# Kernel optimization log

Measured on AMD Instinct MI355X. Metric: run time of the kernel, lower is better.

The kernel has to match this reference:

```python
import jax, jax.numpy as jnp
import numpy as np

B, N, E, K = 8, 4096, 1, 3
F = [16, 32, 16]
MLP_HID, MLP_OUT = 64, 1


def graph_filter(x, S, h, b):
    # x: [B, Fin, N], S: [E, N, N], h: [Fout, E, K, Fin], b: [Fout, 1]
    Bx, Fin, Nx = x.shape
    Ex, Kx = h.shape[1], h.shape[2]
    cur = jnp.broadcast_to(x[:, None], (Bx, Ex, Fin, Nx))  # tap 0: z = x
    zs = [cur]
    for _ in range(Kx - 1):
        cur = jnp.einsum('enm,befm->befn', S, cur)  # diffuse one hop
        zs.append(cur)
    z = jnp.stack(zs, axis=2)  # [B, E, K, Fin, N]
    return jnp.einsum('gekf,bekfn->bgn', h, z) + b[None]  # [B, Fout, N]


def gnn_layer(x, S, h, b, n_out):
    # GraphFilter -> ReLU -> NoPool (select first n_out nodes)
    return jax.nn.relu(graph_filter(x, S, h, b))[:, :, :n_out]


def setup_inputs() -> dict:
    key = jax.random.key(0)
    ks = jax.random.split(key, 16)
    sN = np.float32(1.0 / np.sqrt(N))
    x = jax.random.normal(ks[0], (B, F[0], N), dtype=jnp.float32)
    S_clique = jax.random.normal(ks[1], (E, N, N), dtype=jnp.float32) * sN
    S_line = jax.random.normal(ks[2], (E, N, N), dtype=jnp.float32) * sN

    def w(k, fo, fi):
        s = np.float32(1.0 / np.sqrt(fi * K))
        return jax.random.normal(k, (fo, E, K, fi), dtype=jnp.float32) * s

    Wc1, bc1 = w(ks[3], F[1], F[0]), jnp.zeros((F[1], 1), jnp.float32)
    Wc2, bc2 = w(ks[4], F[2], F[1]), jnp.zeros((F[2], 1), jnp.float32)
    Wl1, bl1 = w(ks[5], F[1], F[0]), jnp.zeros((F[1], 1), jnp.float32)
    Wl2, bl2 = w(ks[6], F[2], F[1]), jnp.zeros((F[2], 1), jnp.float32)
    d_in = N * F[-1]
    Wm1 = jax.random.normal(ks[7], (MLP_HID, d_in), dtype=jnp.float32) * np.float32(1.0 / np.sqrt(d_in))
    bm1 = jnp.zeros((MLP_HID,), jnp.float32)
    Wm2 = jax.random.normal(ks[8], (MLP_OUT, MLP_HID), dtype=jnp.float32) * np.float32(1.0 / np.sqrt(MLP_HID))
    bm2 = jnp.zeros((MLP_OUT,), jnp.float32)
    return {'x': x, 'S_clique': S_clique, 'S_line': S_line,
            'Wc1': Wc1, 'bc1': bc1, 'Wc2': Wc2, 'bc2': bc2,
            'Wl1': Wl1, 'bl1': bl1, 'Wl2': Wl2, 'bl2': bl2,
            'Wm1': Wm1, 'bm1': bm1, 'Wm2': Wm2, 'bm2': bm2}


def reference(x, S_clique, S_line, Wc1, bc1, Wc2, bc2, Wl1, bl1, Wl2, bl2, Wm1, bm1, Wm2, bm2):
    # clique-expansion branch (L=2 layers)
    y = gnn_layer(x, S_clique, Wc1, bc1, N)
    y = gnn_layer(y, S_clique, Wc2, bc2, N)
    # line-expansion branch (L=2 layers)
    y = gnn_layer(y, S_line, Wl1, bl1, N)
    y = gnn_layer(y, S_line, Wl2, bl2, N)
    yFlat = y.reshape(y.shape[0], -1)  # [B, F[-1]*N] (row-major matches torch)
    h = jax.nn.relu(yFlat @ Wm1.T + bm1)
    return h @ Wm2.T + bm2  # [B, 1]
```

## Files before the change

### kernel.cpp

```cpp
#include <hip/hip_runtime.h>


#define NN 4096
#define BB 8

typedef unsigned short u16;
typedef unsigned int   u32;

typedef __attribute__((ext_vector_type(8))) short bf16x8;
typedef __attribute__((ext_vector_type(4))) float f32x4;

__device__ __forceinline__ u16 f2bf(float f) {
    union { float f; u32 i; } c; c.f = f;
    u32 i = c.i;
    u32 r = (i + 0x7FFFu + ((i >> 16) & 1u)) >> 16;
    return (u16)r;
}
__device__ __forceinline__ float bf2f(u16 u) {
    union { u32 i; float f; } c; c.i = ((u32)u) << 16; return c.f;
}

__device__ __forceinline__ void gload_lds16(const u16* g, u16* l) {
    __builtin_amdgcn_global_load_lds(
        (__attribute__((address_space(1))) void*)g,
        (__attribute__((address_space(3))) void*)l, 16, 0, 0);
}

__global__ __launch_bounds__(256) void cvt_f32_bf16(const float* __restrict__ in,
                                                    u16* __restrict__ out, int n)
{
    int i = (blockIdx.x * 256 + threadIdx.x) * 4;
    const int stride = gridDim.x * 256 * 4;
    for (; i < n; i += stride) {
        float4 v = *(const float4*)(in + i);
        ushort4 o;
        o.x = f2bf(v.x); o.y = f2bf(v.y); o.z = f2bf(v.z); o.w = f2bf(v.w);
        *(ushort4*)(out + i) = o;
    }
}

__global__ __launch_bounds__(256) void diffuse(const u16* __restrict__ Z,
                                               const u16* __restrict__ S,
                                               u16* __restrict__ Part)
{
    __shared__ u16 As[2][128 * 64];
    __shared__ u16 Bs[2][64 * 64];

    const int bx    = blockIdx.x;
    const int ntile = ((bx & 7) << 3) | (bx >> 3);
    const int nBase = ntile * 64;
    const int mBase = blockIdx.y * 128;
    const int tid   = threadIdx.x;
    const int lane  = tid & 63;
    const int wv    = tid >> 6;
    const int quad  = lane >> 4;
    const int l16   = lane & 15;

    const int kSlice = NN / (int)gridDim.z;
    const int kStart = (int)blockIdx.z * kSlice;
    const int iters  = kSlice / 64;

    const int rl   = lane >> 3;
    const int gsl  = lane & 7;
    const int gsrc = gsl ^ rl;

    f32x4 acc[2][4];
#pragma unroll
    for (int i = 0; i < 2; ++i)
#pragma unroll
        for (int j = 0; j < 4; ++j) acc[i][j] = (f32x4){0.f, 0.f, 0.f, 0.f};

    auto stage = [&](int buf, int k0) {
#pragma unroll
        for (int j = 0; j < 4; ++j) {
            const int rb = (wv * 4 + j) * 8;
            gload_lds16(Z + (size_t)(mBase + rb + rl) * NN + k0 + gsrc * 8,
                        &As[buf][rb * 64]);
        }
#pragma unroll
        for (int j = 0; j < 2; ++j) {
            const int rb = (wv * 2 + j) * 8;
            gload_lds16(S + (size_t)(nBase + rb + rl) * NN + k0 + gsrc * 8,
                        &Bs[buf][rb * 64]);
        }
    };

    auto compute = [&](int buf) {
#pragma unroll
        for (int s = 0; s < 2; ++s) {
            const int g = s * 4 + quad;
            bf16x8 af[2], bf[4];
#pragma unroll
            for (int mi = 0; mi < 2; ++mi) {
                const int r = wv * 32 + mi * 16 + l16;
                af[mi] = *(const bf16x8*)&As[buf][r * 64 + ((g ^ (r & 7)) << 3)];
            }
#pragma unroll
            for (int ni = 0; ni < 4; ++ni) {
                const int r = ni * 16 + l16;
                bf[ni] = *(const bf16x8*)&Bs[buf][r * 64 + ((g ^ (r & 7)) << 3)];
            }
#pragma unroll
            for (int mi = 0; mi < 2; ++mi)
#pragma unroll
                for (int ni = 0; ni < 4; ++ni)
                    acc[mi][ni] = __builtin_amdgcn_mfma_f32_16x16x32_bf16(
                        af[mi], bf[ni], acc[mi][ni], 0, 0, 0);
        }
    };

    stage(0, kStart);
    __syncthreads();

    int cur = 0;
    for (int i = 0; i < iters - 1; ++i) {
        stage(cur ^ 1, kStart + (i + 1) * 64);
        compute(cur);
        __syncthreads();
        cur ^= 1;
    }
    compute(cur);

    const size_t plane = (size_t)gridDim.y * 128 * NN;
    u16* pp = Part + (size_t)blockIdx.z * plane;
#pragma unroll
    for (int mi = 0; mi < 2; ++mi)
#pragma unroll
        for (int ni = 0; ni < 4; ++ni) {
            const int row0 = mBase + wv * 32 + mi * 16 + quad * 4;
            const int col  = nBase + ni * 16 + l16;
#pragma unroll
            for (int i = 0; i < 4; ++i)
                pp[(size_t)(row0 + i) * NN + col] = f2bf(acc[mi][ni][i]);
        }
}

template <int KS>
__global__ __launch_bounds__(256) void reduce_part(const u16* __restrict__ part,
                                                   int planeElems,
                                                   u16* __restrict__ outb)
{
    const int base   = (blockIdx.x * 256 + threadIdx.x) * 8;
    const int stride = gridDim.x * 256 * 8;
    for (int i = base; i < planeElems; i += stride) {
        float s[8];
#pragma unroll
        for (int e = 0; e < 8; ++e) s[e] = 0.f;
#pragma unroll
        for (int p = 0; p < KS; ++p) {
            uint4 v = *(const uint4*)(part + (size_t)p * planeElems + i);
            const u32 w[4] = {v.x, v.y, v.z, v.w};
#pragma unroll
            for (int q = 0; q < 4; ++q) {
                union { u32 i; float f; } lo, hi;
                lo.i = w[q] << 16;
                hi.i = w[q] & 0xFFFF0000u;
                s[q * 2]     += lo.f;
                s[q * 2 + 1] += hi.f;
            }
        }
        uint4 o;
        o.x = (u32)f2bf(s[0]) | ((u32)f2bf(s[1]) << 16);
        o.y = (u32)f2bf(s[2]) | ((u32)f2bf(s[3]) << 16);
        o.z = (u32)f2bf(s[4]) | ((u32)f2bf(s[5]) << 16);
        o.w = (u32)f2bf(s[6]) | ((u32)f2bf(s[7]) << 16);
        *(uint4*)(outb + i) = o;
    }
}

template <int FIN, int FOUT, int KS>
__global__ __launch_bounds__(256) void combine_relu(
    const u16* __restrict__ z0, const u16* __restrict__ z1,
    const u16* __restrict__ part2, int planeElems,
    const float* __restrict__ W, const float* __restrict__ bias,
    u16* __restrict__ out)
{
    __shared__ float hs[FOUT * 3 * FIN];
    __shared__ float bs[FOUT];
    for (int i = threadIdx.x; i < FOUT * 3 * FIN; i += 256) hs[i] = W[i];
    if (threadIdx.x < FOUT) bs[threadIdx.x] = bias[threadIdx.x];
    __syncthreads();

    const int nb = NN / 256;
    const int b  = blockIdx.x / nb;
    const int n  = (blockIdx.x % nb) * 256 + threadIdx.x;

    float zv[3][FIN];
    const u16* zp0 = z0 + (size_t)b * FIN * NN + n;
    const u16* zp1 = z1 + (size_t)b * FIN * NN + n;
    const u16* zp2 = part2 + (size_t)b * FIN * NN + n;
#pragma unroll
    for (int f = 0; f < FIN; ++f) {
        zv[0][f] = bf2f(zp0[(size_t)f * NN]);
        zv[1][f] = bf2f(zp1[(size_t)f * NN]);
        float s = 0.f;
#pragma unroll
        for (int p = 0; p < KS; ++p)
            s += bf2f(zp2[(size_t)p * planeElems + (size_t)f * NN]);
        zv[2][f] = s;
    }

    u16* op = out + (size_t)b * FOUT * NN + n;
    for (int g = 0; g < FOUT; ++g) {
        float acc = bs[g];
#pragma unroll
        for (int k = 0; k < 3; ++k)
#pragma unroll
            for (int f = 0; f < FIN; ++f)
                acc = fmaf(hs[(g * 3 + k) * FIN + f], zv[k][f], acc);
        op[(size_t)g * NN] = f2bf(fmaxf(acc, 0.f));
    }
}

__global__ __launch_bounds__(256) void mlp1(const u16* __restrict__ y,
                                            const float* __restrict__ Wm1,
                                            float* __restrict__ h1p)
{
    const int j    = blockIdx.x;
    const int base = blockIdx.y * 8192;
    const int D    = 16 * NN;

    float acc[BB];
#pragma unroll
    for (int b = 0; b < BB; ++b) acc[b] = 0.f;

    const float* wrow = Wm1 + (size_t)j * D + base;
    for (int idx = threadIdx.x * 8; idx < 8192; idx += 256 * 8) {
        float4 w0 = *(const float4*)(wrow + idx);
        float4 w1 = *(const float4*)(wrow + idx + 4);
#pragma unroll
        for (int b = 0; b < BB; ++b) {
            uint4 yv = *(const uint4*)(y + (size_t)b * D + base + idx);
            union { u32 i; float f; } c[8];
            c[0].i = yv.x << 16; c[1].i = yv.x & 0xFFFF0000u;
            c[2].i = yv.y << 16; c[3].i = yv.y & 0xFFFF0000u;
            c[4].i = yv.z << 16; c[5].i = yv.z & 0xFFFF0000u;
            c[6].i = yv.w << 16; c[7].i = yv.w & 0xFFFF0000u;
            acc[b] = fmaf(w0.x, c[0].f, acc[b]);
            acc[b] = fmaf(w0.y, c[1].f, acc[b]);
            acc[b] = fmaf(w0.z, c[2].f, acc[b]);
            acc[b] = fmaf(w0.w, c[3].f, acc[b]);
            acc[b] = fmaf(w1.x, c[4].f, acc[b]);
            acc[b] = fmaf(w1.y, c[5].f, acc[b]);
            acc[b] = fmaf(w1.z, c[6].f, acc[b]);
            acc[b] = fmaf(w1.w, c[7].f, acc[b]);
        }
    }

    __shared__ float red[BB][4];
    const int lane = threadIdx.x & 63;
    const int w    = threadIdx.x >> 6;
#pragma unroll
    for (int b = 0; b < BB; ++b) {
        float v = acc[b];
        for (int off = 32; off > 0; off >>= 1) v += __shfl_down(v, off, 64);
        if (lane == 0) red[b][w] = v;
    }
    __syncthreads();
    if (threadIdx.x < BB) {
        const int b = threadIdx.x;
        h1p[blockIdx.y * (BB * 64) + b * 64 + j] =
            red[b][0] + red[b][1] + red[b][2] + red[b][3];
    }
}

__global__ void mlp2(const float* __restrict__ h1p,
                     const float* __restrict__ bm1,
                     const float* __restrict__ Wm2,
                     const float* __restrict__ bm2, float* __restrict__ out)
{
    const int lane = threadIdx.x;
    const float w    = Wm2[lane];
    const float b1   = bm1[lane];
    const float bias = bm2[0];
    for (int b = 0; b < BB; ++b) {
        float h = 0.f;
#pragma unroll
        for (int p = 0; p < 8; ++p) h += h1p[p * (BB * 64) + b * 64 + lane];
        float v = fmaxf(h + b1, 0.f) * w;
        for (int off = 32; off > 0; off >>= 1) v += __shfl_down(v, off, 64);
        if (lane == 0) out[b] = v + bias;
    }
}

extern "C" void kernel_launch(void* const* d_in, const int* in_sizes, int n_in,
                              void* d_out, int out_size, void* d_ws, size_t ws_size,
                              hipStream_t stream)
{
    const float* x   = (const float*)d_in[0];
    const float* Sc  = (const float*)d_in[1];
    const float* Sl  = (const float*)d_in[2];
    const float* Wc1 = (const float*)d_in[3];
    const float* bc1 = (const float*)d_in[4];
    const float* Wc2 = (const float*)d_in[5];
    const float* bc2 = (const float*)d_in[6];
    const float* Wl1 = (const float*)d_in[7];
    const float* bl1 = (const float*)d_in[8];
    const float* Wl2 = (const float*)d_in[9];
    const float* bl2 = (const float*)d_in[10];
    const float* Wm1 = (const float*)d_in[11];
    const float* bm1 = (const float*)d_in[12];
    const float* Wm2 = (const float*)d_in[13];
    const float* bm2 = (const float*)d_in[14];
    float* out = (float*)d_out;

    char* ws = (char*)d_ws;
    u16*   part = (u16*)(ws);
    u16*   zb1  = (u16*)(ws + (8u  << 20));
    u16*   yPa  = (u16*)(ws + (12u << 20));
    u16*   yPb  = (u16*)(ws + (14u << 20));
    float* h1p  = (float*)(ws + (16u << 20));
    u16*   Scb  = (u16*)(ws + (17u << 20));
    u16*   Slb  = Scb + (size_t)NN * NN;

    const dim3 blk(256);
    const dim3 gridCmb(BB * NN / 256);
    const dim3 g2(64, 1, 8);
    const dim3 g4(64, 2, 4);
    const int  pl128 = 128 * NN;
    const int  pl256 = 256 * NN;

    cvt_f32_bf16<<<1024, blk, 0, stream>>>(Sc, Scb, NN * NN);
    cvt_f32_bf16<<<1024, blk, 0, stream>>>(Sl, Slb, NN * NN);
    cvt_f32_bf16<<<512, blk, 0, stream>>>(x, yPa, 128 * NN);

    diffuse<<<g2, blk, 0, stream>>>(yPa, Scb, part);
    reduce_part<8><<<256, blk, 0, stream>>>(part, pl128, zb1);
    diffuse<<<g2, blk, 0, stream>>>(zb1, Scb, part);
    combine_relu<16, 32, 8><<<gridCmb, blk, 0, stream>>>(yPa, zb1, part, pl128,
                                                         Wc1, bc1, yPb);
    diffuse<<<g4, blk, 0, stream>>>(yPb, Scb, part);
    reduce_part<4><<<512, blk, 0, stream>>>(part, pl256, zb1);
    diffuse<<<g4, blk, 0, stream>>>(zb1, Scb, part);
    combine_relu<32, 16, 4><<<gridCmb, blk, 0, stream>>>(yPb, zb1, part, pl256,
                                                         Wc2, bc2, yPa);
    diffuse<<<g2, blk, 0, stream>>>(yPa, Slb, part);
    reduce_part<8><<<256, blk, 0, stream>>>(part, pl128, zb1);
    diffuse<<<g2, blk, 0, stream>>>(zb1, Slb, part);
    combine_relu<16, 32, 8><<<gridCmb, blk, 0, stream>>>(yPa, zb1, part, pl128,
                                                         Wl1, bl1, yPb);
    diffuse<<<g4, blk, 0, stream>>>(yPb, Slb, part);
    reduce_part<4><<<512, blk, 0, stream>>>(part, pl256, zb1);
    diffuse<<<g4, blk, 0, stream>>>(zb1, Slb, part);
    combine_relu<32, 16, 4><<<gridCmb, blk, 0, stream>>>(yPb, zb1, part, pl256,
                                                         Wl2, bl2, yPa);
    mlp1<<<dim3(64, 8), blk, 0, stream>>>(yPa, Wm1, h1p);
    mlp2<<<1, 64, 0, stream>>>(h1p, bm1, Wm2, bm2, out);
}
```

Measured before the change: 388.0 us.

## Triple-buffer diffuse GEMM with vmcnt waits, LDS-staged stores, fused conversions

The diffuse GEMM moves from a double-buffered loop with __syncthreads to a three-stage LDS pipeline. It uses explicit s_waitcnt vmcnt counts and raw barriers, and the iteration count becomes a template parameter so the loop fully unrolls. The output tile is staged through LDS so partial results go out as 16-byte row-contiguous stores instead of scattered 2-byte writes. The three f32-to-bf16 conversion launches are merged into one kernel. The changes aim to hide global-load latency and cut store transactions and launch overhead, at the cost of more LDS per block (possible occupancy loss) and hand-counted waitcnt values that must match the number of issued loads.

After: 373.6 us. 3.7% less time.

```diff
diff --git a/kernel.cpp b/kernel.cpp
--- a/kernel.cpp
+++ b/kernel.cpp
@@ -26,25 +26,31 @@
         (__attribute__((address_space(3))) void*)l, 16, 0, 0);
 }
 
-__global__ __launch_bounds__(256) void cvt_f32_bf16(const float* __restrict__ in,
-                                                    u16* __restrict__ out, int n)
-{
-    int i = (blockIdx.x * 256 + threadIdx.x) * 4;
-    const int stride = gridDim.x * 256 * 4;
-    for (; i < n; i += stride) {
-        float4 v = *(const float4*)(in + i);
+__global__ __launch_bounds__(256) void cvt3(const float* __restrict__ a, u16* __restrict__ da, int na,
+                                            const float* __restrict__ b, u16* __restrict__ db, int nb,
+                                            const float* __restrict__ c, u16* __restrict__ dc, int nc)
+{
+    const int tot = (na + nb + nc) >> 2;
+    for (int q = blockIdx.x * 256 + threadIdx.x; q < tot; q += gridDim.x * 256) {
+        const int i = q << 2;
+        const float* s; u16* d;
+        if (i < na)           { s = a + i;            d = da + i; }
+        else if (i < na + nb) { s = b + (i - na);     d = db + (i - na); }
+        else                  { s = c + (i - na - nb); d = dc + (i - na - nb); }
+        float4 v = *(const float4*)s;
         ushort4 o;
         o.x = f2bf(v.x); o.y = f2bf(v.y); o.z = f2bf(v.z); o.w = f2bf(v.w);
-        *(ushort4*)(out + i) = o;
-    }
-}
-
+        *(ushort4*)d = o;
+    }
+}
+
+template <int ITERS>
 __global__ __launch_bounds__(256) void diffuse(const u16* __restrict__ Z,
                                                const u16* __restrict__ S,
                                                u16* __restrict__ Part)
 {
-    __shared__ u16 As[2][128 * 64];
-    __shared__ u16 Bs[2][64 * 64];
+    __shared__ u16 As[3 * 128 * 64];
+    __shared__ u16 Bs[3 * 64 * 64];
 
     const int bx    = blockIdx.x;
     const int ntile = ((bx & 7) << 3) | (bx >> 3);
@@ -56,9 +62,7 @@
     const int quad  = lane >> 4;
     const int l16   = lane & 15;
 
-    const int kSlice = NN / (int)gridDim.z;
-    const int kStart = (int)blockIdx.z * kSlice;
-    const int iters  = kSlice / 64;
+    const int kStart = (int)blockIdx.z * (ITERS * 64);
 
     const int rl   = lane >> 3;
     const int gsl  = lane & 7;
@@ -75,13 +79,13 @@
         for (int j = 0; j < 4; ++j) {
             const int rb = (wv * 4 + j) * 8;
             gload_lds16(Z + (size_t)(mBase + rb + rl) * NN + k0 + gsrc * 8,
-                        &As[buf][rb * 64]);
+                        &As[buf * 8192 + rb * 64]);
         }
 #pragma unroll
         for (int j = 0; j < 2; ++j) {
             const int rb = (wv * 2 + j) * 8;
             gload_lds16(S + (size_t)(nBase + rb + rl) * NN + k0 + gsrc * 8,
-                        &Bs[buf][rb * 64]);
+                        &Bs[buf * 4096 + rb * 64]);
         }
     };
 
@@ -93,12 +97,12 @@
 #pragma unroll
             for (int mi = 0; mi < 2; ++mi) {
                 const int r = wv * 32 + mi * 16 + l16;
-                af[mi] = *(const bf16x8*)&As[buf][r * 64 + ((g ^ (r & 7)) << 3)];
+                af[mi] = *(const bf16x8*)&As[buf * 8192 + r * 64 + ((g ^ (r & 7)) << 3)];
             }
 #pragma unroll
             for (int ni = 0; ni < 4; ++ni) {
                 const int r = ni * 16 + l16;
-                bf[ni] = *(const bf16x8*)&Bs[buf][r * 64 + ((g ^ (r & 7)) << 3)];
+                bf[ni] = *(const bf16x8*)&Bs[buf * 4096 + r * 64 + ((g ^ (r & 7)) << 3)];
             }
 #pragma unroll
             for (int mi = 0; mi < 2; ++mi)
@@ -110,29 +114,45 @@
     };
 
     stage(0, kStart);
-    __syncthreads();
-
-    int cur = 0;
-    for (int i = 0; i < iters - 1; ++i) {
-        stage(cur ^ 1, kStart + (i + 1) * 64);
-        compute(cur);
-        __syncthreads();
-        cur ^= 1;
-    }
-    compute(cur);
+    stage(1, kStart + 64);
+
+#pragma unroll
+    for (int i = 0; i < ITERS; ++i) {
+        if (i + 2 < ITERS) stage((i + 2) % 3, kStart + (i + 2) * 64);
+        if (i < ITERS - 2)
+            asm volatile("s_waitcnt vmcnt(12)" ::: "memory");
+        else if (i == ITERS - 2)
+            asm volatile("s_waitcnt vmcnt(6)" ::: "memory");
+        else
+            asm volatile("s_waitcnt vmcnt(0)" ::: "memory");
+        __builtin_amdgcn_s_barrier();
+        compute(i % 3);
+        if (i + 1 < ITERS) __builtin_amdgcn_s_barrier();
+    }
+
+    asm volatile("s_waitcnt lgkmcnt(0)" ::: "memory");
+    __builtin_amdgcn_s_barrier();
+
+    u16* tb = &As[wv * 2304];
+#pragma unroll
+    for (int mi = 0; mi < 2; ++mi)
+#pragma unroll
+        for (int ni = 0; ni < 4; ++ni)
+#pragma unroll
+            for (int i = 0; i < 4; ++i)
+                tb[(mi * 16 + quad * 4 + i) * 72 + ni * 16 + l16] =
+                    f2bf(acc[mi][ni][i]);
 
     const size_t plane = (size_t)gridDim.y * 128 * NN;
     u16* pp = Part + (size_t)blockIdx.z * plane;
-#pragma unroll
-    for (int mi = 0; mi < 2; ++mi)
-#pragma unroll
-        for (int ni = 0; ni < 4; ++ni) {
-            const int row0 = mBase + wv * 32 + mi * 16 + quad * 4;
-            const int col  = nBase + ni * 16 + l16;
-#pragma unroll
-            for (int i = 0; i < 4; ++i)
-                pp[(size_t)(row0 + i) * NN + col] = f2bf(acc[mi][ni][i]);
-        }
+    const int row0g = mBase + wv * 32;
+#pragma unroll
+    for (int j = 0; j < 4; ++j) {
+        const int r = (lane >> 3) + j * 8;
+        const int c = (lane & 7) * 8;
+        bf16x8 v = *(const bf16x8*)&tb[r * 72 + c];
+        *(bf16x8*)&pp[(size_t)(row0g + r) * NN + nBase + c] = v;
+    }
 }
 
 template <int KS>
@@ -320,28 +340,27 @@
     const int  pl128 = 128 * NN;
     const int  pl256 = 256 * NN;
 
-    cvt_f32_bf16<<<1024, blk, 0, stream>>>(Sc, Scb, NN * NN);
-    cvt_f32_bf16<<<1024, blk, 0, stream>>>(Sl, Slb, NN * NN);
-    cvt_f32_bf16<<<512, blk, 0, stream>>>(x, yPa, 128 * NN);
-
-    diffuse<<<g2, blk, 0, stream>>>(yPa, Scb, part);
+    cvt3<<<2048, blk, 0, stream>>>(Sc, Scb, NN * NN, Sl, Slb, NN * NN,
+                                   x, yPa, 128 * NN);
+
+    diffuse<8><<<g2, blk, 0, stream>>>(yPa, Scb, part);
     reduce_part<8><<<256, blk, 0, stream>>>(part, pl128, zb1);
-    diffuse<<<g2, blk, 0, stream>>>(zb1, Scb, part);
+    diffuse<8><<<g2, blk, 0, stream>>>(zb1, Scb, part);
     combine_relu<16, 32, 8><<<gridCmb, blk, 0, stream>>>(yPa, zb1, part, pl128,
                                                          Wc1, bc1, yPb);
-    diffuse<<<g4, blk, 0, stream>>>(yPb, Scb, part);
+    diffuse<16><<<g4, blk, 0, stream>>>(yPb, Scb, part);
     reduce_part<4><<<512, blk, 0, stream>>>(part, pl256, zb1);
-    diffuse<<<g4, blk, 0, stream>>>(zb1, Scb, part);
+    diffuse<16><<<g4, blk, 0, stream>>>(zb1, Scb, part);
     combine_relu<32, 16, 4><<<gridCmb, blk, 0, stream>>>(yPb, zb1, part, pl256,
                                                          Wc2, bc2, yPa);
-    diffuse<<<g2, blk, 0, stream>>>(yPa, Slb, part);
+    diffuse<8><<<g2, blk, 0, stream>>>(yPa, Slb, part);
     reduce_part<8><<<256, blk, 0, stream>>>(part, pl128, zb1);
-    diffuse<<<g2, blk, 0, stream>>>(zb1, Slb, part);
+    diffuse<8><<<g2, blk, 0, stream>>>(zb1, Slb, part);
     combine_relu<16, 32, 8><<<gridCmb, blk, 0, stream>>>(yPa, zb1, part, pl128,
                                                          Wl1, bl1, yPb);
-    diffuse<<<g4, blk, 0, stream>>>(yPb, Slb, part);
+    diffuse<16><<<g4, blk, 0, stream>>>(yPb, Slb, part);
     reduce_part<4><<<512, blk, 0, stream>>>(part, pl256, zb1);
-    diffuse<<<g4, blk, 0, stream>>>(zb1, Slb, part);
+    diffuse<16><<<g4, blk, 0, stream>>>(zb1, Slb, part);
     combine_relu<32, 16, 4><<<gridCmb, blk, 0, stream>>>(yPb, zb1, part, pl256,
                                                          Wl2, bl2, yPa);
     mlp1<<<dim3(64, 8), blk, 0, stream>>>(yPa, Wm1, h1p);
```
